# Optimization experiments

Hardware: AMD Instinct MI355X
Metric: run time of the kernel (lower is better)

Reference implementation:

```python
import jax, jax.numpy as jnp
import numpy as np
import math

CHUNK = 32
NS_STEPS = 5
MAX_GNORM = 10.0


def _normalize(x, eps=1e-12):
    n = jnp.linalg.norm(x, axis=-1, keepdims=True)
    return x / jnp.maximum(n, eps)


def _poly(x):  # poly_degree = 2: [x, x^2] / sqrt(2)
    return jnp.concatenate([x, x * x], axis=-1) / math.sqrt(2.0)


def _ns5(G):
    # Muon-style Newton-Schulz orthogonalization (quintic, 5 steps)
    a, b, c = 3.4445, -4.7750, 2.0315
    t = G.shape[0] > G.shape[1]
    X = G.T if t else G
    X = X / (jnp.linalg.norm(X) + 1e-7)
    for _ in range(NS_STEPS):
        A = X @ X.T
        B = b * A + c * (A @ A)
        X = a * X + B @ X
    return X.T if t else X


def _clip_mean(g):
    # per-sample grad-norm clipping to MAX_GNORM, then mean over samples
    n = g.shape[0]
    norms = jnp.maximum(jnp.linalg.norm(g.reshape(n, -1), axis=1), 1e-8)
    scale = jnp.maximum(norms / MAX_GNORM, 1.0)
    return jnp.mean(g / scale.reshape((n,) + (1,) * (g.ndim - 1)), axis=0)


def _mem_fwd(W0, W1, z):  # MemoryMLP depth=2, gelu (exact) between layers
    return jax.nn.gelu(z @ W0, approximate=False) @ W1


def setup_inputs() -> dict:
    key = jax.random.key(0)
    ks = jax.random.split(key, 16)
    B, S, D, M, P, H = 2, 1024, 2048, 512, 1024, 2048
    w = lambda k, shape, fan_in: jax.random.normal(k, shape, jnp.float32) / np.float32(np.sqrt(fan_in))
    return {
        "x": jax.random.normal(ks[0], (B, S, D), jnp.float32),
        "Wk": w(ks[1], (M, D), D),
        "Wv": w(ks[2], (M, D), D),
        "Wq": w(ks[3], (M, D), D),
        "Wout": w(ks[4], (D, M), M),
        "w_lr": w(ks[5], (1, D), D), "b_lr": jnp.full((1,), -4.0, jnp.float32),
        "w_mom": w(ks[6], (1, D), D), "b_mom": jnp.full((1,), 1.0, jnp.float32),
        "w_dec": w(ks[7], (1, D), D), "b_dec": jnp.full((1,), -3.0, jnp.float32),
        "w_gate": w(ks[8], (1, D), D), "b_gate": jnp.full((1,), -1.0, jnp.float32),
        "Wmem0": w(ks[9], (P, H), P),
        "Wmem1": w(ks[10], (H, P), H),
        "Wmemout": w(ks[11], (P, M), P),
        "Wvexp": w(ks[12], (M, P), M),
    }


def reference(x, Wk, Wv, Wq, Wout, w_lr, b_lr, w_mom, b_mom, w_dec, b_dec,
              w_gate, b_gate, Wmem0, Wmem1, Wmemout, Wvexp):
    # Inference path (torch.is_grad_enabled() == False): chunked ATLAS update.
    B, S, D = x.shape
    NC = S // CHUNK

    k = _normalize(x @ Wk.T)          # (B,S,M)
    v = x @ Wv.T                       # (B,S,M)
    q = _normalize(x @ Wq.T)          # (B,S,M)
    kp = _poly(k)                      # (B,S,P)
    qp = _poly(q)                      # (B,S,P)
    vexp = v @ Wvexp                   # v_expand: (B,S,P)

    gate = lambda w, b: jax.nn.sigmoid(jnp.einsum('bsd,od->bso', x, w) + b)
    lr, mom, dec, og = gate(w_lr, b_lr), gate(w_mom, b_mom), gate(w_dec, b_dec), gate(w_gate, b_gate)

    cmean = lambda t: t[..., 0].reshape(B, NC, CHUNK).mean(axis=(0, 2))  # per-chunk scalar
    lr_c, mom_c, dec_c = cmean(lr), cmean(mom), cmean(dec)

    chunks = lambda t: t.reshape(B, NC, CHUNK, t.shape[-1]).transpose(1, 0, 2, 3)  # (NC,B,C,F)
    qc, kc, vc = chunks(qp), chunks(kp), chunks(vexp)

    def loss_fn(params, kk, vv):  # ||M(k) - v||^2 per sample
        W0_, W1_ = params
        pred = jax.nn.gelu(kk @ W0_, approximate=False) @ W1_
        return jnp.sum((pred - vv) ** 2)

    grad_fn = jax.vmap(jax.grad(loss_fn), in_axes=((None, None), 0, 0))

    def step(carry, xs):
        W0, W1, S0, S1 = carry
        qch, kch, vch, lrc, momc, decc = xs
        retr = _mem_fwd(W0, W1, qch) @ Wmemout  # retrieve with pre-update params: (B,C,M)
        kf = kch.reshape(-1, kch.shape[-1])
        vf = vch.reshape(-1, vch.shape[-1])
        g0, g1 = grad_fn((W0, W1), kf, vf)      # per-sample grads
        g0, g1 = _clip_mean(g0), _clip_mean(g1)
        s0 = momc * S0 - lrc * g0                # surprise momentum
        s1 = momc * S1 - lrc * g1
        W0n = (1.0 - decc) * W0 + _ns5(s0) * lrc # forget gate + orthogonalized step
        W1n = (1.0 - decc) * W1 + _ns5(s1) * lrc
        return (W0n, W1n, s0, s1), retr

    init = (Wmem0, Wmem1, jnp.zeros_like(Wmem0), jnp.zeros_like(Wmem1))
    _, retrs = jax.lax.scan(step, init, (qc, kc, vc, lr_c, mom_c, dec_c))
    retrieved = retrs.transpose(1, 0, 2, 3).reshape(B, S, -1)  # (B,S,M)
    delta = retrieved @ Wout.T
    return x + delta * og
```

## Files before the change

kernel.cpp:

```cpp
#include <hip/hip_runtime.h>


typedef unsigned short us;
typedef __attribute__((ext_vector_type(8))) short s16x8;
typedef __attribute__((ext_vector_type(8))) unsigned short u16x8;
typedef __attribute__((ext_vector_type(4))) float f32x4;

#define MKP 72

__device__ __forceinline__ float gelu_f(float x) {
  return 0.5f * x * (1.0f + erff(x * 0.70710678118654752f));
}
__device__ __forceinline__ float gelu_grad_f(float x) {
  float cdf = 0.5f * (1.0f + erff(x * 0.70710678118654752f));
  float pdf = 0.3989422804014327f * expf(-0.5f * x * x);
  return cdf + x * pdf;
}
__device__ __forceinline__ float sigmoid_f(float x) { return 1.0f / (1.0f + expf(-x)); }

__device__ __forceinline__ us f2bf(float f) {
  union { float f; unsigned u; } v; v.f = f;
  unsigned r = (v.u + 0x7FFFu + ((v.u >> 16) & 1u)) >> 16;
  return (us)r;
}
__device__ __forceinline__ float bf2f(us h) {
  union { unsigned u; float f; } v; v.u = ((unsigned)h) << 16;
  return v.f;
}
__device__ __forceinline__ int cm_map(int n) {
  return ((n & 1023) >> 5) * 64 + (n >> 10) * 32 + (n & 31);
}

__device__ __forceinline__ float block_reduce_sum(float v, float* red) {
  int t = threadIdx.x;
  red[t] = v; __syncthreads();
  for (int s = blockDim.x >> 1; s > 0; s >>= 1) {
    if (t < s) red[t] += red[t + s];
    __syncthreads();
  }
  float r = red[0];
  __syncthreads();
  return r;
}

template<int EPI, int TA, int DUAL, int AG>
__global__ __launch_bounds__(64)
void mg_k(const us* __restrict__ Aq, const us* __restrict__ A2,
          const us* __restrict__ Bq, void* __restrict__ Cq,
          void* __restrict__ C2, const void* __restrict__ Eq,
          const float* __restrict__ FX, const float* __restrict__ OG,
          const float* __restrict__ cp, int cidx,
          int M, int N, int K, int lda, int ldb, int ldc, int lde,
          float c1, float c2, long sA, long sB, long sC, long sE) {
  __shared__ __align__(16) us As[64 * MKP];
  __shared__ __align__(16) us Bs[64 * MKP];
  const int bz = blockIdx.z;
  const us* A = Aq + (size_t)bz * sA;
  const us* B = Bq + (size_t)bz * sB;
  const int t = threadIdx.x;
  const int m0 = blockIdx.y * 64, n0 = blockIdx.x * 64;
  if constexpr (DUAL) { if (m0 >= 64) A = A2; }
  const int mA0 = DUAL ? (m0 & 63) : m0;
  const int l15 = t & 15, l4 = t >> 4;

  f32x4 acc[4][4];
#pragma unroll
  for (int i = 0; i < 4; ++i)
#pragma unroll
    for (int j = 0; j < 4; ++j) acc[i][j] = (f32x4){0.f, 0.f, 0.f, 0.f};

  const int srw = t >> 3;
  const int sck = (t & 7) * 8;

  u16x8 ra[8], rb[8];
  auto LDA = [&](int k0) {
#pragma unroll
    for (int p = 0; p < 8; ++p) {
      if constexpr (TA == 0) {
        int row = srw + p * 8;
        int srow;
        if constexpr (AG) srow = cm_map(m0 + row); else srow = mA0 + row;
        ra[p] = *(const u16x8*)(A + (size_t)srow * lda + k0 + sck);
      } else {
        ra[p] = *(const u16x8*)(A + (size_t)(k0 + srw + p * 8) * lda + mA0 + sck);
      }
    }
  };
  auto LDB = [&](int k0) {
#pragma unroll
    for (int p = 0; p < 8; ++p)
      rb[p] = *(const u16x8*)(B + (size_t)(n0 + srw + p * 8) * ldb + k0 + sck);
  };

  LDA(0); LDB(0);
  for (int k0 = 0; k0 < K; k0 += 64) {
    if constexpr (TA == 0) {
#pragma unroll
      for (int p = 0; p < 8; ++p)
        *(u16x8*)&As[(srw + p * 8) * MKP + sck] = ra[p];
    } else {
#pragma unroll
      for (int p = 0; p < 8; ++p) {
        int kk = srw + p * 8;
#pragma unroll
        for (int j = 0; j < 8; ++j) As[(sck + j) * MKP + kk] = ra[p][j];
      }
    }
#pragma unroll
    for (int p = 0; p < 8; ++p)
      *(u16x8*)&Bs[(srw + p * 8) * MKP + sck] = rb[p];
    if (k0 + 64 < K) { LDA(k0 + 64); LDB(k0 + 64); }
#pragma unroll
    for (int ks = 0; ks < 2; ++ks) {
      s16x8 af[4], bf[4];
#pragma unroll
      for (int mi = 0; mi < 4; ++mi)
        af[mi] = *(const s16x8*)&As[(mi * 16 + l15) * MKP + ks * 32 + l4 * 8];
#pragma unroll
      for (int ni = 0; ni < 4; ++ni)
        bf[ni] = *(const s16x8*)&Bs[(ni * 16 + l15) * MKP + ks * 32 + l4 * 8];
#pragma unroll
      for (int mi = 0; mi < 4; ++mi)
#pragma unroll
        for (int ni = 0; ni < 4; ++ni)
          acc[mi][ni] = __builtin_amdgcn_mfma_f32_16x16x32_bf16(af[mi], bf[ni], acc[mi][ni], 0, 0, 0);
    }
  }

#pragma unroll
  for (int mi = 0; mi < 4; ++mi) {
#pragma unroll
    for (int i = 0; i < 4; ++i) {
      int grow = m0 + mi * 16 + l4 * 4 + i;
#pragma unroll
      for (int ni = 0; ni < 4; ++ni) {
        int col = n0 + ni * 16 + l15;
        float v = acc[mi][ni][i];
        if constexpr (EPI == 5) {
          ((us*)Cq + bz * sC)[(size_t)grow * ldc + col] = f2bf(v);
        } else if constexpr (EPI == 6) {
          const us* E = (const us*)Eq + bz * sE;
          ((us*)Cq + bz * sC)[(size_t)grow * ldc + col] =
              f2bf(c1 * v + c2 * bf2f(E[(size_t)grow * lde + col]));
        } else if constexpr (EPI == 7) {
          ((float*)Cq)[(size_t)grow * ldc + col] = v;
        } else if constexpr (EPI == 8) {
          ((us*)Cq)[(size_t)grow * ldc + col] = f2bf(gelu_f(v));
          if (m0 >= 64)
            ((float*)C2)[(size_t)(grow - 64) * ldc + col] = gelu_grad_f(v);
        } else if constexpr (EPI == 9) {
          if (m0 < 64)
            ((us*)Cq)[(size_t)grow * ldc + col] = f2bf(v);
          else
            ((us*)Cq)[(size_t)grow * ldc + col] =
                f2bf(2.0f * (v - ((const float*)Eq)[(size_t)(grow - 64) * lde + col]));
        } else if constexpr (EPI == 13) {
          ((float*)Cq)[(size_t)grow * ldc + col] =
              v * ((const float*)Eq)[(size_t)grow * lde + col];
        } else if constexpr (EPI == 14) {
          float* C = (float*)Cq;
          float old = C[(size_t)grow * ldc + col];
          C[(size_t)grow * ldc + col] = cp[cidx * 3 + 1] * old - cp[cidx * 3 + 0] * v;
        } else if constexpr (EPI == 15) {
          ((float*)Cq)[(size_t)grow * ldc + col] =
              FX[(size_t)grow * ldc + col] + v * OG[grow];
        } else if constexpr (EPI == 17) {
          int crow = cm_map(grow);
          ((float*)Cq)[(size_t)crow * ldc + col] = v;
        }
      }
    }
  }
}

template<int EPI, int TA = 0, int DUAL = 0, int AG = 0>
static void mg(hipStream_t st, const us* A, const us* A2, const us* B,
               void* C, void* C2, const void* E,
               const float* FX, const float* OG, const float* cp, int cidx,
               int M, int N, int K, int lda, int ldb, int ldc, int lde,
               float c1, float c2, long sA, long sB, long sC, long sE, int batch) {
  dim3 g(N / 64, M / 64, batch), b(64);
  hipLaunchKernelGGL((mg_k<EPI, TA, DUAL, AG>), g, b, 0, st, A, A2, B, C, C2, E,
                     FX, OG, cp, cidx, M, N, K, lda, ldb, ldc, lde, c1, c2, sA, sB, sC, sE);
}


__global__ __launch_bounds__(256) void conv_k(const float* __restrict__ in,
                                              us* __restrict__ out, int n) {
  for (int i = blockIdx.x * 256 + threadIdx.x; i < n; i += gridDim.x * 256)
    out[i] = f2bf(in[i]);
}

__global__ void tconv_k(const float* __restrict__ in, us* __restrict__ out, int R, int C) {
  __shared__ float tile[32][33];
  int c0 = blockIdx.x * 32, r0 = blockIdx.y * 32;
  int tx = threadIdx.x, ty = threadIdx.y;
#pragma unroll
  for (int j = 0; j < 4; ++j)
    tile[ty + 8 * j][tx] = in[(size_t)(r0 + ty + 8 * j) * C + c0 + tx];
  __syncthreads();
#pragma unroll
  for (int j = 0; j < 4; ++j)
    out[(size_t)(c0 + ty + 8 * j) * R + r0 + tx] = f2bf(tile[tx][ty + 8 * j]);
}


__global__ __launch_bounds__(256) void polynorm2_k(const float* __restrict__ lin,
                                                   us* __restrict__ outp) {
  __shared__ float red[256];
  int n = blockIdx.x, t = threadIdx.x;
  int rowp = cm_map(n);
  float s = 0.f;
  for (int f = t; f < 512; f += 256) { float v = lin[(size_t)n * 512 + f]; s += v * v; }
  float tot = block_reduce_sum(s, red);
  float sc = 1.0f / fmaxf(sqrtf(tot), 1e-12f);
  const float is2 = 0.70710678118654752f;
  for (int f = t; f < 512; f += 256) {
    float v = lin[(size_t)n * 512 + f] * sc;
    outp[(size_t)rowp * 1024 + f] = f2bf(v * is2);
    outp[(size_t)rowp * 1024 + 512 + f] = f2bf(v * v * is2);
  }
}

__global__ __launch_bounds__(256) void gates_k(const float* __restrict__ x,
    const float* __restrict__ wlr, const float* __restrict__ blr,
    const float* __restrict__ wmom, const float* __restrict__ bmom,
    const float* __restrict__ wdec, const float* __restrict__ bdec,
    const float* __restrict__ wgate, const float* __restrict__ bgate,
    float* __restrict__ lrv, float* __restrict__ momv,
    float* __restrict__ decv, float* __restrict__ og) {
  __shared__ float red[256];
  int n = blockIdx.x, t = threadIdx.x;
  float s0 = 0.f, s1 = 0.f, s2 = 0.f, s3 = 0.f;
  for (int d = t; d < 2048; d += 256) {
    float xv = x[(size_t)n * 2048 + d];
    s0 += xv * wlr[d]; s1 += xv * wmom[d]; s2 += xv * wdec[d]; s3 += xv * wgate[d];
  }
  float r0 = block_reduce_sum(s0, red);
  float r1 = block_reduce_sum(s1, red);
  float r2 = block_reduce_sum(s2, red);
  float r3 = block_reduce_sum(s3, red);
  if (t == 0) {
    lrv[n] = sigmoid_f(r0 + blr[0]);
    momv[n] = sigmoid_f(r1 + bmom[0]);
    decv[n] = sigmoid_f(r2 + bdec[0]);
    og[n] = sigmoid_f(r3 + bgate[0]);
  }
}

__global__ void chunk_means_k(const float* __restrict__ lrv, const float* __restrict__ momv,
                              const float* __restrict__ decv, float* __restrict__ cp) {
  int c = blockIdx.x, t = threadIdx.x;
  int n = ((t >> 5) << 10) + c * 32 + (t & 31);
  float a = lrv[n], b = momv[n], d = decv[n];
  for (int off = 32; off > 0; off >>= 1) {
    a += __shfl_down(a, off);
    b += __shfl_down(b, off);
    d += __shfl_down(d, off);
  }
  if (t == 0) {
    cp[c * 3 + 0] = a * (1.f / 64.f);
    cp[c * 3 + 1] = b * (1.f / 64.f);
    cp[c * 3 + 2] = d * (1.f / 64.f);
  }
}

__global__ __launch_bounds__(256) void sampnorm2_k(const us* __restrict__ kp_b,
                                                   const float* __restrict__ dh,
                                                   const us* __restrict__ hab,
                                                   const us* __restrict__ pr,
                                                   float* __restrict__ w0inv,
                                                   float* __restrict__ w1inv, int c) {
  __shared__ float red[256];
  int i = blockIdx.x, t = threadIdx.x;
  int row = c * 64 + i;
  float sk = 0.f, sr = 0.f, sdh = 0.f, sa = 0.f;
  for (int p = t; p < 1024; p += 256) {
    float v = bf2f(kp_b[(size_t)row * 1024 + p]); sk += v * v;
    v = bf2f(pr[(size_t)(64 + i) * 1024 + p]); sr += v * v;
  }
  for (int h = t; h < 2048; h += 256) {
    float v = dh[(size_t)i * 2048 + h]; sdh += v * v;
    v = bf2f(hab[(size_t)(64 + i) * 2048 + h]); sa += v * v;
  }
  float tk = block_reduce_sum(sk, red);
  float tdh = block_reduce_sum(sdh, red);
  float ta = block_reduce_sum(sa, red);
  float tr = block_reduce_sum(sr, red);
  if (t == 0) {
    float n0 = fmaxf(sqrtf(tk) * sqrtf(tdh), 1e-8f);
    w0inv[i] = 1.0f / (64.0f * fmaxf(n0 * 0.1f, 1.0f));
    float n1 = fmaxf(sqrtf(ta) * sqrtf(tr), 1e-8f);
    w1inv[i] = 1.0f / (64.0f * fmaxf(n1 * 0.1f, 1.0f));
  }
}

template<int INF32>
__global__ void wtrans_k(const void* __restrict__ in, const float* __restrict__ w,
                         us* __restrict__ out, int C, int ldin) {
  __shared__ float tile[32][33];
  int c0 = blockIdx.x * 32, r0 = blockIdx.y * 32;
  int tx = threadIdx.x, ty = threadIdx.y;
#pragma unroll
  for (int j = 0; j < 4; ++j) {
    int r = r0 + ty + 8 * j, cc = c0 + tx;
    float v;
    if constexpr (INF32) v = ((const float*)in)[(size_t)r * ldin + cc];
    else v = bf2f(((const us*)in)[(size_t)r * ldin + cc]);
    tile[ty + 8 * j][tx] = v * w[r];
  }
  __syncthreads();
#pragma unroll
  for (int j = 0; j < 4; ++j)
    out[(size_t)(c0 + ty + 8 * j) * 64 + r0 + tx] = f2bf(tile[tx][ty + 8 * j]);
}

__global__ __launch_bounds__(256) void frob2_k(const float* __restrict__ s0,
                                               const float* __restrict__ s1, int n,
                                               float* __restrict__ parts) {
  __shared__ float red[256];
  const float* s = blockIdx.z ? s1 : s0;
  float acc = 0.f;
  for (int i = blockIdx.x * 256 + threadIdx.x; i < n; i += gridDim.x * 256) {
    float v = s[i]; acc += v * v;
  }
  float r = block_reduce_sum(acc, red);
  if (threadIdx.x == 0) parts[blockIdx.z * 256 + blockIdx.x] = r;
}

__global__ __launch_bounds__(256) void frob_fin2_k(const float* __restrict__ parts,
                                                   float* __restrict__ inv) {
  __shared__ float red[256];
  float r = block_reduce_sum(parts[blockIdx.x * 256 + threadIdx.x], red);
  if (threadIdx.x == 0) inv[blockIdx.x] = 1.0f / (sqrtf(r) + 1e-7f);
}

__global__ void scale_dual_k(const float* __restrict__ in, us* __restrict__ outS,
                             us* __restrict__ outT, const float* __restrict__ inv,
                             int R, int C) {
  __shared__ float tile[32][33];
  float s = *inv;
  int c0 = blockIdx.x * 32, r0 = blockIdx.y * 32;
  int tx = threadIdx.x, ty = threadIdx.y;
#pragma unroll
  for (int j = 0; j < 4; ++j) {
    float v = in[(size_t)(r0 + ty + 8 * j) * C + c0 + tx];
    tile[ty + 8 * j][tx] = v;
    outS[(size_t)(r0 + ty + 8 * j) * C + c0 + tx] = f2bf(v * s);
  }
  __syncthreads();
#pragma unroll
  for (int j = 0; j < 4; ++j)
    outT[(size_t)(c0 + ty + 8 * j) * R + r0 + tx] = f2bf(tile[tx][ty + 8 * j] * s);
}

__global__ void tbf_k(const us* __restrict__ in, us* __restrict__ out) {
  __shared__ us tile[32][33];
  size_t bo = (size_t)blockIdx.z * 2097152;
  int c0 = blockIdx.x * 32, r0 = blockIdx.y * 32;
  int tx = threadIdx.x, ty = threadIdx.y;
#pragma unroll
  for (int j = 0; j < 4; ++j)
    tile[ty + 8 * j][tx] = in[bo + (size_t)(r0 + ty + 8 * j) * 2048 + c0 + tx];
  __syncthreads();
#pragma unroll
  for (int j = 0; j < 4; ++j)
    out[bo + (size_t)(c0 + ty + 8 * j) * 1024 + r0 + tx] = tile[tx][ty + 8 * j];
}

__global__ void wupd0_k(float* __restrict__ W0, const us* __restrict__ X,
                        us* __restrict__ W0bT, const float* __restrict__ cp, int c) {
  __shared__ float tl[32][33];
  float lr = cp[c * 3 + 0], om = 1.0f - cp[c * 3 + 2];
  int c0 = blockIdx.x * 32, r0 = blockIdx.y * 32;
  int tx = threadIdx.x, ty = threadIdx.y;
#pragma unroll
  for (int j = 0; j < 4; ++j) {
    int r = r0 + ty + 8 * j, h = c0 + tx;
    size_t idx = (size_t)r * 2048 + h;
    float v = om * W0[idx] + lr * bf2f(X[idx]);
    W0[idx] = v;
    tl[ty + 8 * j][tx] = v;
  }
  __syncthreads();
#pragma unroll
  for (int j = 0; j < 4; ++j)
    W0bT[(size_t)(c0 + ty + 8 * j) * 1024 + r0 + tx] = f2bf(tl[tx][ty + 8 * j]);
}

__global__ void wupd1_k(float* __restrict__ W1, const us* __restrict__ X2,
                        us* __restrict__ W1b, us* __restrict__ W1bT,
                        const float* __restrict__ cp, int c) {
  __shared__ float tX[32][33];
  __shared__ float t2[32][33];
  float lr = cp[c * 3 + 0], om = 1.0f - cp[c * 3 + 2];
  int h0 = blockIdx.x * 32, p0 = blockIdx.y * 32;
  int tx = threadIdx.x, ty = threadIdx.y;
#pragma unroll
  for (int j = 0; j < 4; ++j)
    tX[ty + 8 * j][tx] = bf2f(X2[(size_t)(p0 + ty + 8 * j) * 2048 + h0 + tx]);
  __syncthreads();
#pragma unroll
  for (int j = 0; j < 4; ++j) {
    int h = h0 + ty + 8 * j, p = p0 + tx;
    size_t idx = (size_t)h * 1024 + p;
    float v = om * W1[idx] + lr * tX[tx][ty + 8 * j];
    W1[idx] = v;
    W1b[idx] = f2bf(v);
    t2[tx][ty + 8 * j] = v;
  }
  __syncthreads();
#pragma unroll
  for (int j = 0; j < 4; ++j)
    W1bT[(size_t)(p0 + ty + 8 * j) * 2048 + h0 + tx] = f2bf(t2[ty + 8 * j][tx]);
}


extern "C" void kernel_launch(void* const* d_in, const int* in_sizes, int n_in,
                              void* d_out, int out_size, void* d_ws, size_t ws_size,
                              hipStream_t stream) {
  const float* x = (const float*)d_in[0];
  const float* Wk = (const float*)d_in[1];
  const float* Wv = (const float*)d_in[2];
  const float* Wq = (const float*)d_in[3];
  const float* Wout = (const float*)d_in[4];
  const float* w_lr = (const float*)d_in[5];
  const float* b_lr = (const float*)d_in[6];
  const float* w_mom = (const float*)d_in[7];
  const float* b_mom = (const float*)d_in[8];
  const float* w_dec = (const float*)d_in[9];
  const float* b_dec = (const float*)d_in[10];
  const float* w_gate = (const float*)d_in[11];
  const float* b_gate = (const float*)d_in[12];
  const float* Wmem0 = (const float*)d_in[13];
  const float* Wmem1 = (const float*)d_in[14];
  const float* Wmemout = (const float*)d_in[15];
  const float* Wvexp = (const float*)d_in[16];
  float* out = (float*)d_out;
  (void)n_in; (void)in_sizes; (void)out_size;

  const long F = 1048576;
  const long BIG = 2097152;
  const long SB2 = 2097152, SB1 = 1048576;
  float* ws = (float*)d_ws;
  if (ws_size < (size_t)25043464 * sizeof(float)) return;

  us* kp_b   = (us*)ws;
  us* qp_b   = (us*)(ws + F);
  float* vexp = ws + 2 * F;
  float* W0  = ws + 4 * F;
  float* W1  = ws + 6 * F;
  float* S0  = ws + 8 * F;
  float* S1  = ws + 10 * F;
  us* XA     = (us*)(ws + 12 * F);
  us* XB     = (us*)(ws + 14 * F);
  us* XT     = (us*)(ws + 16 * F);
  us* Ab     = (us*)(ws + 18 * F);
  float* SCR = ws + 19 * F;
  us* W0bT   = (us*)(ws + 20 * F);
  us* W1bT   = (us*)(ws + 21 * F);
  us* W1b    = (us*)(ws + 22 * F);
  us* WmoT   = (us*)(ws + 23 * F);
  us* retrv  = (us*)(ws + 23 * F + 262144);
  float* smal = ws + 23 * F + 262144 + 524288;
  float* og   = smal;
  float* lrv  = og + 2048;
  float* momv = lrv + 2048;
  float* decv = momv + 2048;
  float* cpb  = decv + 2048;
  float* w0inv = cpb + 128;
  float* w1inv = w0inv + 64;
  float* parts = w1inv + 64;
  float* inv01 = parts + 512;

  us* xb   = XA;
  us* Wkb  = XB;
  us* Wqb  = XB + 1048576;
  us* Wvb  = XB + 2097152;
  us* vlin = XT;
  us* WvexpT = XT + 1048576;
  us* Woutb = Ab;
  float* lin = SCR;
  us* Bb = (us*)SCR;
  us* hab   = (us*)SCR;
  float* gp = SCR + 131072;
  us* pr    = (us*)(SCR + 262144);
  float* dh = SCR + 327680;
  us* dhT   = (us*)(SCR + 458752);
  us* rbwT  = (us*)(SCR + 524288);

  const float NSa = 3.4445f, NSb = -4.7750f, NSc = 2.0315f;

  hipMemcpyAsync(W0, Wmem0, (size_t)BIG * 4, hipMemcpyDeviceToDevice, stream);
  hipMemcpyAsync(W1, Wmem1, (size_t)BIG * 4, hipMemcpyDeviceToDevice, stream);
  hipMemsetAsync(S0, 0, (size_t)BIG * 4, stream);
  hipMemsetAsync(S1, 0, (size_t)BIG * 4, stream);
  hipLaunchKernelGGL(tconv_k, dim3(64, 32), dim3(32, 8), 0, stream, Wmem0, W0bT, 1024, 2048);
  hipLaunchKernelGGL(conv_k, dim3(1024), dim3(256), 0, stream, Wmem1, W1b, (int)BIG);
  hipLaunchKernelGGL(tconv_k, dim3(32, 64), dim3(32, 8), 0, stream, Wmem1, W1bT, 2048, 1024);
  hipLaunchKernelGGL(tconv_k, dim3(16, 32), dim3(32, 8), 0, stream, Wmemout, WmoT, 1024, 512);
  hipLaunchKernelGGL(tconv_k, dim3(32, 16), dim3(32, 8), 0, stream, Wvexp, WvexpT, 512, 1024);
  hipLaunchKernelGGL(conv_k, dim3(2048), dim3(256), 0, stream, x, xb, 2048 * 2048);
  hipLaunchKernelGGL(conv_k, dim3(512), dim3(256), 0, stream, Wk, Wkb, 512 * 2048);
  hipLaunchKernelGGL(conv_k, dim3(512), dim3(256), 0, stream, Wq, Wqb, 512 * 2048);
  hipLaunchKernelGGL(conv_k, dim3(512), dim3(256), 0, stream, Wv, Wvb, 512 * 2048);

  mg<7>(stream, xb, nullptr, Wkb, lin, nullptr, nullptr, nullptr, nullptr, nullptr, 0,
        2048, 512, 2048, 2048, 2048, 512, 0, 0.f, 0.f, 0, 0, 0, 0, 1);
  hipLaunchKernelGGL(polynorm2_k, dim3(2048), dim3(256), 0, stream, lin, kp_b);
  mg<7>(stream, xb, nullptr, Wqb, lin, nullptr, nullptr, nullptr, nullptr, nullptr, 0,
        2048, 512, 2048, 2048, 2048, 512, 0, 0.f, 0.f, 0, 0, 0, 0, 1);
  hipLaunchKernelGGL(polynorm2_k, dim3(2048), dim3(256), 0, stream, lin, qp_b);
  mg<5>(stream, xb, nullptr, Wvb, vlin, nullptr, nullptr, nullptr, nullptr, nullptr, 0,
        2048, 512, 2048, 2048, 2048, 512, 0, 0.f, 0.f, 0, 0, 0, 0, 1);
  mg<17>(stream, vlin, nullptr, WvexpT, vexp, nullptr, nullptr, nullptr, nullptr, nullptr, 0,
         2048, 1024, 512, 512, 512, 1024, 0, 0.f, 0.f, 0, 0, 0, 0, 1);

  hipLaunchKernelGGL(gates_k, dim3(2048), dim3(256), 0, stream, x,
                     w_lr, b_lr, w_mom, b_mom, w_dec, b_dec, w_gate, b_gate,
                     lrv, momv, decv, og);
  hipLaunchKernelGGL(chunk_means_k, dim3(32), dim3(64), 0, stream, lrv, momv, decv, cpb);

  for (int c = 0; c < 32; ++c) {
    const us* kp_c = kp_b + (size_t)c * 64 * 1024;
    const us* qp_c = qp_b + (size_t)c * 64 * 1024;
    const float* vexp_c = vexp + (size_t)c * 64 * 1024;
    mg<8, 0, 1>(stream, qp_c, kp_c, W0bT, hab, gp, nullptr, nullptr, nullptr, nullptr, 0,
                128, 2048, 1024, 1024, 1024, 2048, 0, 0.f, 0.f, 0, 0, 0, 0, 1);
    mg<9>(stream, hab, nullptr, W1bT, pr, nullptr, vexp_c, nullptr, nullptr, nullptr, 0,
          128, 1024, 2048, 2048, 2048, 1024, 1024, 0.f, 0.f, 0, 0, 0, 0, 1);
    mg<5>(stream, pr, nullptr, WmoT, retrv + (size_t)c * 64 * 512, nullptr, nullptr,
          nullptr, nullptr, nullptr, 0,
          64, 512, 1024, 1024, 1024, 512, 0, 0.f, 0.f, 0, 0, 0, 0, 1);
    mg<13>(stream, pr + 64 * 1024, nullptr, W1b, dh, nullptr, gp, nullptr, nullptr, nullptr, 0,
           64, 2048, 1024, 1024, 1024, 2048, 2048, 0.f, 0.f, 0, 0, 0, 0, 1);
    hipLaunchKernelGGL(sampnorm2_k, dim3(64), dim3(256), 0, stream,
                       kp_b, dh, hab, pr, w0inv, w1inv, c);
    hipLaunchKernelGGL((wtrans_k<1>), dim3(64, 2), dim3(32, 8), 0, stream, dh, w0inv, dhT, 2048, 2048);
    hipLaunchKernelGGL((wtrans_k<0>), dim3(32, 2), dim3(32, 8), 0, stream, pr + 64 * 1024, w1inv,
                       rbwT, 1024, 1024);
    mg<14, 1>(stream, kp_c, nullptr, dhT, S0, nullptr, nullptr, nullptr, nullptr, cpb, c,
              1024, 2048, 64, 1024, 64, 2048, 0, 0.f, 0.f, 0, 0, 0, 0, 1);
    mg<14, 1>(stream, hab + 64 * 2048, nullptr, rbwT, S1, nullptr, nullptr, nullptr, nullptr, cpb, c,
              2048, 1024, 64, 2048, 64, 1024, 0, 0.f, 0.f, 0, 0, 0, 0, 1);

    hipLaunchKernelGGL(frob2_k, dim3(256, 1, 2), dim3(256), 0, stream, S0, S1, (int)BIG, parts);
    hipLaunchKernelGGL(frob_fin2_k, dim3(2), dim3(256), 0, stream, parts, inv01);
    hipLaunchKernelGGL(scale_dual_k, dim3(64, 32), dim3(32, 8), 0, stream,
                       S0, XA, XT, inv01, 1024, 2048);
    hipLaunchKernelGGL(scale_dual_k, dim3(32, 64), dim3(32, 8), 0, stream,
                       S1, XT + SB2, XA + SB2, inv01 + 1, 2048, 1024);

    us* Xc = XA;
    us* Xn = XB;
    for (int it = 0; it < 5; ++it) {
      mg<5>(stream, Xc, nullptr, Xc, Ab, nullptr, nullptr, nullptr, nullptr, nullptr, 0,
            1024, 1024, 2048, 2048, 2048, 1024, 0, 0.f, 0.f, SB2, SB2, SB1, 0, 2);
      mg<6>(stream, Ab, nullptr, Ab, Bb, nullptr, Ab, nullptr, nullptr, nullptr, 0,
            1024, 1024, 1024, 1024, 1024, 1024, 1024, NSc, NSb, SB1, SB1, SB1, SB1, 2);
      mg<6>(stream, Bb, nullptr, XT, Xn, nullptr, Xc, nullptr, nullptr, nullptr, 0,
            1024, 2048, 1024, 1024, 1024, 2048, 2048, 1.0f, NSa, SB1, SB2, SB2, SB2, 2);
      if (it < 4)
        hipLaunchKernelGGL(tbf_k, dim3(64, 32, 2), dim3(32, 8), 0, stream, Xn, XT);
      us* tmp = Xc; Xc = Xn; Xn = tmp;
    }
    hipLaunchKernelGGL(wupd0_k, dim3(64, 32), dim3(32, 8), 0, stream, W0, Xc, W0bT, cpb, c);
    hipLaunchKernelGGL(wupd1_k, dim3(64, 32), dim3(32, 8), 0, stream, W1, Xc + SB2, W1b, W1bT, cpb, c);
  }

  hipLaunchKernelGGL(conv_k, dim3(1024), dim3(256), 0, stream, Wout, Woutb, 2048 * 512);
  mg<15, 0, 0, 1>(stream, retrv, nullptr, Woutb, out, nullptr, nullptr, x, og, nullptr, 0,
                  2048, 2048, 512, 512, 512, 2048, 0, 0.f, 0.f, 0, 0, 0, 0, 1);
}
```

Baseline: 16.89 ms.

## Pre-pack Newton-Schulz operands into MFMA fragment layout and skip LDS staging

Adds a packed tile layout (`pf_off`) that stores 16x32 bf16 blocks in exactly the per-lane order the MFMA 16x16x32 instruction consumes. A new GEMM kernel (`mgf_k`) for the Newton-Schulz iterations loads A/B fragments straight from global memory into registers, double-buffered, with no shared-memory round trip. The producer kernels (`scalepk_k`, `packX_k`, and the GEMM epilogues) now write X, X^T, A and B in this packed form. The goal is to remove LDS stores, loads and transposes from the dominant orthogonalization GEMMs. The cost is extra packing work in the epilogues and reliance on L2 for operand reuse. The packed buffers also reuse workspace regions shared with W0bT and W1b, which are rebuilt at the end of each chunk.

```diff
diff --git a/kernel.cpp b/kernel.cpp
--- a/kernel.cpp
+++ b/kernel.cpp
@@ -29,6 +29,9 @@
 }
 __device__ __forceinline__ int cm_map(int n) {
   return ((n & 1023) >> 5) * 64 + (n >> 10) * 32 + (n & 31);
+}
+__device__ __forceinline__ size_t pf_off(int r, int k, int KB) {
+  return ((size_t)(r >> 4) * KB + (k >> 5)) * 512 + ((k >> 3) & 3) * 128 + (r & 15) * 8 + (k & 7);
 }
 
 __device__ __forceinline__ float block_reduce_sum(float v, float* red) {
@@ -43,25 +46,30 @@
   return r;
 }
 
-template<int EPI, int TA, int DUAL, int AG>
+template<int EPI>
 __global__ __launch_bounds__(64)
-void mg_k(const us* __restrict__ Aq, const us* __restrict__ A2,
-          const us* __restrict__ Bq, void* __restrict__ Cq,
-          void* __restrict__ C2, const void* __restrict__ Eq,
-          const float* __restrict__ FX, const float* __restrict__ OG,
-          const float* __restrict__ cp, int cidx,
-          int M, int N, int K, int lda, int ldb, int ldc, int lde,
-          float c1, float c2, long sA, long sB, long sC, long sE) {
-  __shared__ __align__(16) us As[64 * MKP];
-  __shared__ __align__(16) us Bs[64 * MKP];
+void mgf_k(const us* __restrict__ Apf, const us* __restrict__ Bpf,
+           us* __restrict__ Cq, const us* __restrict__ Eq,
+           int M, int N, int K, int ldc,
+           float c1, float c2, long sA, long sB, long sC, long sE) {
+  __shared__ __align__(16) us ct[4096];
   const int bz = blockIdx.z;
-  const us* A = Aq + (size_t)bz * sA;
-  const us* B = Bq + (size_t)bz * sB;
-  const int t = threadIdx.x;
+  const us* A = Apf + (size_t)bz * sA;
+  const us* B = Bpf + (size_t)bz * sB;
+  us* C = Cq + (size_t)bz * sC;
+  const us* E = Eq + (size_t)bz * sE;
+  const int lane = threadIdx.x;
   const int m0 = blockIdx.y * 64, n0 = blockIdx.x * 64;
-  if constexpr (DUAL) { if (m0 >= 64) A = A2; }
-  const int mA0 = DUAL ? (m0 & 63) : m0;
-  const int l15 = t & 15, l4 = t >> 4;
+  const int KB = K >> 5;
+  const int l15 = lane & 15, l4 = lane >> 4;
+
+  const us* am[4];
+  const us* bm[4];
+#pragma unroll
+  for (int q = 0; q < 4; ++q) {
+    am[q] = A + ((size_t)((m0 >> 4) + q) * KB) * 512 + lane * 8;
+    bm[q] = B + ((size_t)((n0 >> 4) + q) * KB) * 512 + lane * 8;
+  }
 
   f32x4 acc[4][4];
 #pragma unroll
@@ -69,64 +77,101 @@
 #pragma unroll
     for (int j = 0; j < 4; ++j) acc[i][j] = (f32x4){0.f, 0.f, 0.f, 0.f};
 
-  const int srw = t >> 3;
-  const int sck = (t & 7) * 8;
-
-  u16x8 ra[8], rb[8];
-  auto LDA = [&](int k0) {
-#pragma unroll
-    for (int p = 0; p < 8; ++p) {
-      if constexpr (TA == 0) {
-        int row = srw + p * 8;
-        int srow;
-        if constexpr (AG) srow = cm_map(m0 + row); else srow = mA0 + row;
-        ra[p] = *(const u16x8*)(A + (size_t)srow * lda + k0 + sck);
+  u16x8 a0[4], b0[4], a1[4], b1[4];
+#pragma unroll
+  for (int q = 0; q < 4; ++q) {
+    a0[q] = *(const u16x8*)(am[q]);
+    b0[q] = *(const u16x8*)(bm[q]);
+    a1[q] = *(const u16x8*)(am[q] + 512);
+    b1[q] = *(const u16x8*)(bm[q] + 512);
+  }
+
+  for (int kb = 0; kb < KB; kb += 2) {
+#pragma unroll
+    for (int mi = 0; mi < 4; ++mi)
+#pragma unroll
+      for (int ni = 0; ni < 4; ++ni)
+        acc[mi][ni] = __builtin_amdgcn_mfma_f32_16x16x32_bf16(
+            (s16x8)a0[mi], (s16x8)b0[ni], acc[mi][ni], 0, 0, 0);
+    if (kb + 2 < KB) {
+#pragma unroll
+      for (int q = 0; q < 4; ++q) {
+        a0[q] = *(const u16x8*)(am[q] + (size_t)(kb + 2) * 512);
+        b0[q] = *(const u16x8*)(bm[q] + (size_t)(kb + 2) * 512);
+      }
+    }
+#pragma unroll
+    for (int mi = 0; mi < 4; ++mi)
+#pragma unroll
+      for (int ni = 0; ni < 4; ++ni)
+        acc[mi][ni] = __builtin_amdgcn_mfma_f32_16x16x32_bf16(
+            (s16x8)a1[mi], (s16x8)b1[ni], acc[mi][ni], 0, 0, 0);
+    if (kb + 3 < KB) {
+#pragma unroll
+      for (int q = 0; q < 4; ++q) {
+        a1[q] = *(const u16x8*)(am[q] + (size_t)(kb + 3) * 512);
+        b1[q] = *(const u16x8*)(bm[q] + (size_t)(kb + 3) * 512);
+      }
+    }
+  }
+
+  if constexpr (EPI == 6) {
+#pragma unroll
+    for (int mi = 0; mi < 4; ++mi) {
+#pragma unroll
+      for (int i = 0; i < 4; ++i) {
+        int grow = m0 + mi * 16 + l4 * 4 + i;
+#pragma unroll
+        for (int ni = 0; ni < 4; ++ni) {
+          int col = n0 + ni * 16 + l15;
+          float v = acc[mi][ni][i];
+          C[(size_t)grow * ldc + col] =
+              f2bf(c1 * v + c2 * bf2f(E[(size_t)grow * ldc + col]));
+        }
+      }
+    }
+  } else {
+#pragma unroll
+    for (int mi = 0; mi < 4; ++mi)
+#pragma unroll
+      for (int i = 0; i < 4; ++i)
+#pragma unroll
+        for (int ni = 0; ni < 4; ++ni)
+          ct[(mi * 16 + l4 * 4 + i) * 64 + ni * 16 + l15] = f2bf(acc[mi][ni][i]);
+    const int KC = N >> 5;
+#pragma unroll
+    for (int q = 0; q < 8; ++q) {
+      int cid = lane * 8 + q;
+      int r = cid >> 3, kc = cid & 7;
+      u16x8 v = *(const u16x8*)&ct[r * 64 + kc * 8];
+      size_t off = pf_off(m0 + r, n0 + kc * 8, KC);
+      if constexpr (EPI == 21) {
+        u16x8 e = *(const u16x8*)(E + off);
+        u16x8 o;
+#pragma unroll
+        for (int w = 0; w < 8; ++w) o[w] = f2bf(c1 * bf2f(v[w]) + c2 * bf2f(e[w]));
+        *(u16x8*)(C + off) = o;
       } else {
-        ra[p] = *(const u16x8*)(A + (size_t)(k0 + srw + p * 8) * lda + mA0 + sck);
+        *(u16x8*)(C + off) = v;
       }
     }
-  };
-  auto LDB = [&](int k0) {
-#pragma unroll
-    for (int p = 0; p < 8; ++p)
-      rb[p] = *(const u16x8*)(B + (size_t)(n0 + srw + p * 8) * ldb + k0 + sck);
-  };
-
-  LDA(0); LDB(0);
-  for (int k0 = 0; k0 < K; k0 += 64) {
-    if constexpr (TA == 0) {
-#pragma unroll
-      for (int p = 0; p < 8; ++p)
-        *(u16x8*)&As[(srw + p * 8) * MKP + sck] = ra[p];
-    } else {
-#pragma unroll
-      for (int p = 0; p < 8; ++p) {
-        int kk = srw + p * 8;
-#pragma unroll
-        for (int j = 0; j < 8; ++j) As[(sck + j) * MKP + kk] = ra[p][j];
-      }
-    }
-#pragma unroll
-    for (int p = 0; p < 8; ++p)
-      *(u16x8*)&Bs[(srw + p * 8) * MKP + sck] = rb[p];
-    if (k0 + 64 < K) { LDA(k0 + 64); LDB(k0 + 64); }
-#pragma unroll
-    for (int ks = 0; ks < 2; ++ks) {
-      s16x8 af[4], bf[4];
-#pragma unroll
-      for (int mi = 0; mi < 4; ++mi)
-        af[mi] = *(const s16x8*)&As[(mi * 16 + l15) * MKP + ks * 32 + l4 * 8];
-#pragma unroll
-      for (int ni = 0; ni < 4; ++ni)
-        bf[ni] = *(const s16x8*)&Bs[(ni * 16 + l15) * MKP + ks * 32 + l4 * 8];
-#pragma unroll
-      for (int mi = 0; mi < 4; ++mi)
-#pragma unroll
-        for (int ni = 0; ni < 4; ++ni)
-          acc[mi][ni] = __builtin_amdgcn_mfma_f32_16x16x32_bf16(af[mi], bf[ni], acc[mi][ni], 0, 0, 0);
-    }
-  }
-
+  }
+}
+
+template<int EPI>
+static void mgf(hipStream_t st, const us* A, const us* B, us* C, const us* E,
+                int M, int N, int K, int ldc, float c1, float c2,
+                long sA, long sB, long sC, long sE) {
+  dim3 g(N / 64, M / 64, 2), b(64);
+  hipLaunchKernelGGL((mgf_k<EPI>), g, b, 0, st, A, B, C, E, M, N, K, ldc,
+                     c1, c2, sA, sB, sC, sE);
+}
+
+template<int EPI>
+__device__ __forceinline__ void epilogue(f32x4 (&acc)[4][4], int m0, int n0,
+    int l15, int l4, void* Cq, void* C2, const void* Eq,
+    const float* FX, const float* OG, const float* cp, int cidx,
+    int ldc, int lde, float c1, float c2) {
 #pragma unroll
   for (int mi = 0; mi < 4; ++mi) {
 #pragma unroll
@@ -137,11 +182,7 @@
         int col = n0 + ni * 16 + l15;
         float v = acc[mi][ni][i];
         if constexpr (EPI == 5) {
-          ((us*)Cq + bz * sC)[(size_t)grow * ldc + col] = f2bf(v);
-        } else if constexpr (EPI == 6) {
-          const us* E = (const us*)Eq + bz * sE;
-          ((us*)Cq + bz * sC)[(size_t)grow * ldc + col] =
-              f2bf(c1 * v + c2 * bf2f(E[(size_t)grow * lde + col]));
+          ((us*)Cq)[(size_t)grow * ldc + col] = f2bf(v);
         } else if constexpr (EPI == 7) {
           ((float*)Cq)[(size_t)grow * ldc + col] = v;
         } else if constexpr (EPI == 8) {
@@ -173,15 +214,173 @@
   }
 }
 
+template<int EPI, int TA, int DUAL, int AG>
+__global__ __launch_bounds__(64)
+void mg_k(const us* __restrict__ Aq, const us* __restrict__ A2,
+          const us* __restrict__ Bq, void* __restrict__ Cq,
+          void* __restrict__ C2, const void* __restrict__ Eq,
+          const float* __restrict__ FX, const float* __restrict__ OG,
+          const float* __restrict__ cp, int cidx,
+          int M, int N, int K, int lda, int ldb, int ldc, int lde,
+          float c1, float c2) {
+  __shared__ __align__(16) us As[64 * MKP];
+  __shared__ __align__(16) us Bs[64 * MKP];
+  const us* A = Aq;
+  const us* B = Bq;
+  const int t = threadIdx.x;
+  const int m0 = blockIdx.y * 64, n0 = blockIdx.x * 64;
+  if constexpr (DUAL) { if (m0 >= 64) A = A2; }
+  const int mA0 = DUAL ? (m0 & 63) : m0;
+  const int l15 = t & 15, l4 = t >> 4;
+
+  f32x4 acc[4][4];
+#pragma unroll
+  for (int i = 0; i < 4; ++i)
+#pragma unroll
+    for (int j = 0; j < 4; ++j) acc[i][j] = (f32x4){0.f, 0.f, 0.f, 0.f};
+
+  const int srw = t >> 3;
+  const int sck = (t & 7) * 8;
+
+  u16x8 ra[8], rb[8];
+  auto LDA = [&](int k0) {
+#pragma unroll
+    for (int p = 0; p < 8; ++p) {
+      if constexpr (TA == 0) {
+        int row = srw + p * 8;
+        int srow;
+        if constexpr (AG) srow = cm_map(m0 + row); else srow = mA0 + row;
+        ra[p] = *(const u16x8*)(A + (size_t)srow * lda + k0 + sck);
+      } else {
+        ra[p] = *(const u16x8*)(A + (size_t)(k0 + srw + p * 8) * lda + mA0 + sck);
+      }
+    }
+  };
+  auto LDB = [&](int k0) {
+#pragma unroll
+    for (int p = 0; p < 8; ++p)
+      rb[p] = *(const u16x8*)(B + (size_t)(n0 + srw + p * 8) * ldb + k0 + sck);
+  };
+
+  LDA(0); LDB(0);
+  for (int k0 = 0; k0 < K; k0 += 64) {
+    if constexpr (TA == 0) {
+#pragma unroll
+      for (int p = 0; p < 8; ++p)
+        *(u16x8*)&As[(srw + p * 8) * MKP + sck] = ra[p];
+    } else {
+#pragma unroll
+      for (int p = 0; p < 8; ++p) {
+        int kk = srw + p * 8;
+#pragma unroll
+        for (int j = 0; j < 8; ++j) As[(sck + j) * MKP + kk] = ra[p][j];
+      }
+    }
+#pragma unroll
+    for (int p = 0; p < 8; ++p)
+      *(u16x8*)&Bs[(srw + p * 8) * MKP + sck] = rb[p];
+    if (k0 + 64 < K) { LDA(k0 + 64); LDB(k0 + 64); }
+#pragma unroll
+    for (int ks = 0; ks < 2; ++ks) {
+      s16x8 af[4], bf[4];
+#pragma unroll
+      for (int mi = 0; mi < 4; ++mi)
+        af[mi] = *(const s16x8*)&As[(mi * 16 + l15) * MKP + ks * 32 + l4 * 8];
+#pragma unroll
+      for (int ni = 0; ni < 4; ++ni)
+        bf[ni] = *(const s16x8*)&Bs[(ni * 16 + l15) * MKP + ks * 32 + l4 * 8];
+#pragma unroll
+      for (int mi = 0; mi < 4; ++mi)
+#pragma unroll
+        for (int ni = 0; ni < 4; ++ni)
+          acc[mi][ni] = __builtin_amdgcn_mfma_f32_16x16x32_bf16(af[mi], bf[ni], acc[mi][ni], 0, 0, 0);
+    }
+  }
+
+  epilogue<EPI>(acc, m0, n0, l15, l4, Cq, C2, Eq, FX, OG, cp, cidx,
+                ldc, lde, c1, c2);
+}
+
 template<int EPI, int TA = 0, int DUAL = 0, int AG = 0>
 static void mg(hipStream_t st, const us* A, const us* A2, const us* B,
                void* C, void* C2, const void* E,
                const float* FX, const float* OG, const float* cp, int cidx,
                int M, int N, int K, int lda, int ldb, int ldc, int lde,
-               float c1, float c2, long sA, long sB, long sC, long sE, int batch) {
-  dim3 g(N / 64, M / 64, batch), b(64);
+               float c1 = 0.f, float c2 = 0.f) {
+  dim3 g(N / 64, M / 64, 1), b(64);
   hipLaunchKernelGGL((mg_k<EPI, TA, DUAL, AG>), g, b, 0, st, A, A2, B, C, C2, E,
-                     FX, OG, cp, cidx, M, N, K, lda, ldb, ldc, lde, c1, c2, sA, sB, sC, sE);
+                     FX, OG, cp, cidx, M, N, K, lda, ldb, ldc, lde, c1, c2);
+}
+
+template<int TR>
+__global__ void scalepk_k(const float* __restrict__ S, const float* __restrict__ inv,
+                          us* __restrict__ Xrm, us* __restrict__ XP,
+                          us* __restrict__ XTP, int R, int C) {
+  __shared__ float tile[32][33];
+  float s = *inv;
+  int c0 = blockIdx.x * 32, r0 = blockIdx.y * 32;
+  int tx = threadIdx.x, ty = threadIdx.y;
+#pragma unroll
+  for (int j = 0; j < 4; ++j)
+    tile[ty + 8 * j][tx] = S[(size_t)(r0 + ty + 8 * j) * C + c0 + tx] * s;
+  __syncthreads();
+  int t = ty * 32 + tx;
+  if (t < 128) {
+    int rh = t >> 2, cc = t & 3;
+    u16x8 v;
+#pragma unroll
+    for (int e = 0; e < 8; ++e) v[e] = f2bf(tile[rh][cc * 8 + e]);
+    int grow = r0 + rh, gcol = c0 + cc * 8;
+    size_t offD = pf_off(grow, gcol, C >> 5);
+    if constexpr (TR == 0) {
+      *(u16x8*)(XP + offD) = v;
+      *(u16x8*)(Xrm + (size_t)grow * C + gcol) = v;
+    } else {
+      *(u16x8*)(XTP + offD) = v;
+    }
+  } else {
+    int ch = (t - 128) >> 2, rc = (t - 128) & 3;
+    u16x8 v;
+#pragma unroll
+    for (int e = 0; e < 8; ++e) v[e] = f2bf(tile[rc * 8 + e][ch]);
+    int trow = c0 + ch, tcol = r0 + rc * 8;
+    size_t offT = pf_off(trow, tcol, R >> 5);
+    if constexpr (TR == 0) {
+      *(u16x8*)(XTP + offT) = v;
+    } else {
+      *(u16x8*)(XP + offT) = v;
+      *(u16x8*)(Xrm + (size_t)trow * R + tcol) = v;
+    }
+  }
+}
+
+__global__ void packX_k(const us* __restrict__ Xn, us* __restrict__ XP,
+                        us* __restrict__ XTP) {
+  __shared__ us tile[32][33];
+  const long SB2c = 2097152;
+  size_t bo = (size_t)blockIdx.z * SB2c;
+  int c0 = blockIdx.x * 32, r0 = blockIdx.y * 32;
+  int tx = threadIdx.x, ty = threadIdx.y;
+#pragma unroll
+  for (int j = 0; j < 4; ++j)
+    tile[ty + 8 * j][tx] = Xn[bo + (size_t)(r0 + ty + 8 * j) * 2048 + c0 + tx];
+  __syncthreads();
+  int t = ty * 32 + tx;
+  if (t < 128) {
+    int rh = t >> 2, cc = t & 3;
+    u16x8 v;
+#pragma unroll
+    for (int e = 0; e < 8; ++e) v[e] = tile[rh][cc * 8 + e];
+    size_t offD = pf_off(r0 + rh, c0 + cc * 8, 64);
+    *(u16x8*)(XP + bo + offD) = v;
+  } else {
+    int ch = (t - 128) >> 2, rc = (t - 128) & 3;
+    u16x8 v;
+#pragma unroll
+    for (int e = 0; e < 8; ++e) v[e] = tile[rc * 8 + e][ch];
+    size_t offT = pf_off(c0 + ch, r0 + rc * 8, 32);
+    *(u16x8*)(XTP + bo + offT) = v;
+  }
 }
 
 
@@ -333,39 +532,6 @@
   __shared__ float red[256];
   float r = block_reduce_sum(parts[blockIdx.x * 256 + threadIdx.x], red);
   if (threadIdx.x == 0) inv[blockIdx.x] = 1.0f / (sqrtf(r) + 1e-7f);
-}
-
-__global__ void scale_dual_k(const float* __restrict__ in, us* __restrict__ outS,
-                             us* __restrict__ outT, const float* __restrict__ inv,
-                             int R, int C) {
-  __shared__ float tile[32][33];
-  float s = *inv;
-  int c0 = blockIdx.x * 32, r0 = blockIdx.y * 32;
-  int tx = threadIdx.x, ty = threadIdx.y;
-#pragma unroll
-  for (int j = 0; j < 4; ++j) {
-    float v = in[(size_t)(r0 + ty + 8 * j) * C + c0 + tx];
-    tile[ty + 8 * j][tx] = v;
-    outS[(size_t)(r0 + ty + 8 * j) * C + c0 + tx] = f2bf(v * s);
-  }
-  __syncthreads();
-#pragma unroll
-  for (int j = 0; j < 4; ++j)
-    outT[(size_t)(c0 + ty + 8 * j) * R + r0 + tx] = f2bf(tile[tx][ty + 8 * j] * s);
-}
-
-__global__ void tbf_k(const us* __restrict__ in, us* __restrict__ out) {
-  __shared__ us tile[32][33];
-  size_t bo = (size_t)blockIdx.z * 2097152;
-  int c0 = blockIdx.x * 32, r0 = blockIdx.y * 32;
-  int tx = threadIdx.x, ty = threadIdx.y;
-#pragma unroll
-  for (int j = 0; j < 4; ++j)
-    tile[ty + 8 * j][tx] = in[bo + (size_t)(r0 + ty + 8 * j) * 2048 + c0 + tx];
-  __syncthreads();
-#pragma unroll
-  for (int j = 0; j < 4; ++j)
-    out[bo + (size_t)(c0 + ty + 8 * j) * 1024 + r0 + tx] = tile[tx][ty + 8 * j];
 }
 
 __global__ void wupd0_k(float* __restrict__ W0, const us* __restrict__ X,
@@ -454,9 +620,11 @@
   float* S1  = ws + 10 * F;
   us* XA     = (us*)(ws + 12 * F);
   us* XB     = (us*)(ws + 14 * F);
-  us* XT     = (us*)(ws + 16 * F);
-  us* Ab     = (us*)(ws + 18 * F);
+  us* XP     = (us*)(ws + 16 * F);
+  us* AP     = (us*)(ws + 18 * F);
   float* SCR = ws + 19 * F;
+  us* XTP    = (us*)(ws + 20 * F);
+  us* BP     = (us*)(ws + 22 * F);
   us* W0bT   = (us*)(ws + 20 * F);
   us* W1bT   = (us*)(ws + 21 * F);
   us* W1b    = (us*)(ws + 22 * F);
@@ -477,11 +645,10 @@
   us* Wkb  = XB;
   us* Wqb  = XB + 1048576;
   us* Wvb  = XB + 2097152;
-  us* vlin = XT;
-  us* WvexpT = XT + 1048576;
-  us* Woutb = Ab;
+  us* vlin = XP;
+  us* WvexpT = XP + 1048576;
+  us* Woutb = AP;
   float* lin = SCR;
-  us* Bb = (us*)SCR;
   us* hab   = (us*)SCR;
   float* gp = SCR + 131072;
   us* pr    = (us*)(SCR + 262144);
@@ -506,15 +673,15 @@
   hipLaunchKernelGGL(conv_k, dim3(512), dim3(256), 0, stream, Wv, Wvb, 512 * 2048);
 
   mg<7>(stream, xb, nullptr, Wkb, lin, nullptr, nullptr, nullptr, nullptr, nullptr, 0,
-        2048, 512, 2048, 2048, 2048, 512, 0, 0.f, 0.f, 0, 0, 0, 0, 1);
+        2048, 512, 2048, 2048, 2048, 512, 0);
   hipLaunchKernelGGL(polynorm2_k, dim3(2048), dim3(256), 0, stream, lin, kp_b);
   mg<7>(stream, xb, nullptr, Wqb, lin, nullptr, nullptr, nullptr, nullptr, nullptr, 0,
-        2048, 512, 2048, 2048, 2048, 512, 0, 0.f, 0.f, 0, 0, 0, 0, 1);
+        2048, 512, 2048, 2048, 2048, 512, 0);
   hipLaunchKernelGGL(polynorm2_k, dim3(2048), dim3(256), 0, stream, lin, qp_b);
   mg<5>(stream, xb, nullptr, Wvb, vlin, nullptr, nullptr, nullptr, nullptr, nullptr, 0,
-        2048, 512, 2048, 2048, 2048, 512, 0, 0.f, 0.f, 0, 0, 0, 0, 1);
+        2048, 512, 2048, 2048, 2048, 512, 0);
   mg<17>(stream, vlin, nullptr, WvexpT, vexp, nullptr, nullptr, nullptr, nullptr, nullptr, 0,
-         2048, 1024, 512, 512, 512, 1024, 0, 0.f, 0.f, 0, 0, 0, 0, 1);
+         2048, 1024, 512, 512, 512, 1024, 0);
 
   hipLaunchKernelGGL(gates_k, dim3(2048), dim3(256), 0, stream, x,
                      w_lr, b_lr, w_mom, b_mom, w_dec, b_dec, w_gate, b_gate,
@@ -526,42 +693,41 @@
     const us* qp_c = qp_b + (size_t)c * 64 * 1024;
     const float* vexp_c = vexp + (size_t)c * 64 * 1024;
     mg<8, 0, 1>(stream, qp_c, kp_c, W0bT, hab, gp, nullptr, nullptr, nullptr, nullptr, 0,
-                128, 2048, 1024, 1024, 1024, 2048, 0, 0.f, 0.f, 0, 0, 0, 0, 1);
+                128, 2048, 1024, 1024, 1024, 2048, 0);
     mg<9>(stream, hab, nullptr, W1bT, pr, nullptr, vexp_c, nullptr, nullptr, nullptr, 0,
-          128, 1024, 2048, 2048, 2048, 1024, 1024, 0.f, 0.f, 0, 0, 0, 0, 1);
+          128, 1024, 2048, 2048, 2048, 1024, 1024);
     mg<5>(stream, pr, nullptr, WmoT, retrv + (size_t)c * 64 * 512, nullptr, nullptr,
-          nullptr, nullptr, nullptr, 0,
-          64, 512, 1024, 1024, 1024, 512, 0, 0.f, 0.f, 0, 0, 0, 0, 1);
+          nullptr, nullptr, nullptr, 0, 64, 512, 1024, 1024, 1024, 512, 0);
     mg<13>(stream, pr + 64 * 1024, nullptr, W1b, dh, nullptr, gp, nullptr, nullptr, nullptr, 0,
-           64, 2048, 1024, 1024, 1024, 2048, 2048, 0.f, 0.f, 0, 0, 0, 0, 1);
+           64, 2048, 1024, 1024, 1024, 2048, 2048);
     hipLaunchKernelGGL(sampnorm2_k, dim3(64), dim3(256), 0, stream,
                        kp_b, dh, hab, pr, w0inv, w1inv, c);
     hipLaunchKernelGGL((wtrans_k<1>), dim3(64, 2), dim3(32, 8), 0, stream, dh, w0inv, dhT, 2048, 2048);
     hipLaunchKernelGGL((wtrans_k<0>), dim3(32, 2), dim3(32, 8), 0, stream, pr + 64 * 1024, w1inv,
                        rbwT, 1024, 1024);
     mg<14, 1>(stream, kp_c, nullptr, dhT, S0, nullptr, nullptr, nullptr, nullptr, cpb, c,
-              1024, 2048, 64, 1024, 64, 2048, 0, 0.f, 0.f, 0, 0, 0, 0, 1);
+              1024, 2048, 64, 1024, 64, 2048, 0);
     mg<14, 1>(stream, hab + 64 * 2048, nullptr, rbwT, S1, nullptr, nullptr, nullptr, nullptr, cpb, c,
-              2048, 1024, 64, 2048, 64, 1024, 0, 0.f, 0.f, 0, 0, 0, 0, 1);
+              2048, 1024, 64, 2048, 64, 1024, 0);
 
     hipLaunchKernelGGL(frob2_k, dim3(256, 1, 2), dim3(256), 0, stream, S0, S1, (int)BIG, parts);
     hipLaunchKernelGGL(frob_fin2_k, dim3(2), dim3(256), 0, stream, parts, inv01);
-    hipLaunchKernelGGL(scale_dual_k, dim3(64, 32), dim3(32, 8), 0, stream,
-                       S0, XA, XT, inv01, 1024, 2048);
-    hipLaunchKernelGGL(scale_dual_k, dim3(32, 64), dim3(32, 8), 0, stream,
-                       S1, XT + SB2, XA + SB2, inv01 + 1, 2048, 1024);
+    hipLaunchKernelGGL((scalepk_k<0>), dim3(64, 32), dim3(32, 8), 0, stream,
+                       S0, inv01, XA, XP, XTP, 1024, 2048);
+    hipLaunchKernelGGL((scalepk_k<1>), dim3(32, 64), dim3(32, 8), 0, stream,
+                       S1, inv01 + 1, XA + SB2, XP + SB2, XTP + SB2, 2048, 1024);
 
     us* Xc = XA;
     us* Xn = XB;
     for (int it = 0; it < 5; ++it) {
-      mg<5>(stream, Xc, nullptr, Xc, Ab, nullptr, nullptr, nullptr, nullptr, nullptr, 0,
-            1024, 1024, 2048, 2048, 2048, 1024, 0, 0.f, 0.f, SB2, SB2, SB1, 0, 2);
-      mg<6>(stream, Ab, nullptr, Ab, Bb, nullptr, Ab, nullptr, nullptr, nullptr, 0,
-            1024, 1024, 1024, 1024, 1024, 1024, 1024, NSc, NSb, SB1, SB1, SB1, SB1, 2);
-      mg<6>(stream, Bb, nullptr, XT, Xn, nullptr, Xc, nullptr, nullptr, nullptr, 0,
-            1024, 2048, 1024, 1024, 1024, 2048, 2048, 1.0f, NSa, SB1, SB2, SB2, SB2, 2);
+      mgf<20>(stream, XP, XP, AP, nullptr, 1024, 1024, 2048, 0,
+              0.f, 0.f, SB2, SB2, SB1, 0);
+      mgf<21>(stream, AP, AP, BP, AP, 1024, 1024, 1024, 0,
+              NSc, NSb, SB1, SB1, SB1, SB1);
+      mgf<6>(stream, BP, XTP, Xn, Xc, 1024, 2048, 1024, 2048,
+             1.0f, NSa, SB1, SB2, SB2, SB2);
       if (it < 4)
-        hipLaunchKernelGGL(tbf_k, dim3(64, 32, 2), dim3(32, 8), 0, stream, Xn, XT);
+        hipLaunchKernelGGL(packX_k, dim3(64, 32, 2), dim3(32, 8), 0, stream, Xn, XP, XTP);
       us* tmp = Xc; Xc = Xn; Xn = tmp;
     }
     hipLaunchKernelGGL(wupd0_k, dim3(64, 32), dim3(32, 8), 0, stream, W0, Xc, W0bT, cpb, c);
@@ -570,5 +736,5 @@
 
   hipLaunchKernelGGL(conv_k, dim3(1024), dim3(256), 0, stream, Wout, Woutb, 2048 * 512);
   mg<15, 0, 0, 1>(stream, retrv, nullptr, Woutb, out, nullptr, nullptr, x, og, nullptr, 0,
-                  2048, 2048, 512, 512, 512, 2048, 0, 0.f, 0.f, 0, 0, 0, 0, 1);
-}
+                  2048, 2048, 512, 512, 512, 2048, 0);
+}
```

Result: no change. 17.16 ms (+1.6%).
